# Kernel optimization log

Hardware: AMD Instinct MI355X
Metric: run time of the kernel (lower is better)

## Reference

```python
import jax, jax.numpy as jnp
import numpy as np

B, N, D_IN, D_OUT = 4, 512, 128, 64
TEMP = 1.0
BN_EPS = 1e-5


def setup_inputs() -> dict:
    key = jax.random.key(0)
    ks = jax.random.split(key, 9)
    return {
        "x": jax.random.normal(ks[0], (B, N, D_IN), jnp.float32),
        "att_proj_w": jax.random.normal(ks[1], (D_OUT, D_IN), jnp.float32) * 0.08,
        "att_proj_b": jax.random.normal(ks[2], (D_OUT,), jnp.float32) * 0.01,
        "att_weight": jax.random.normal(ks[3], (D_OUT, 1), jnp.float32) * 0.15,
        "proj_with_att_w": jax.random.normal(ks[4], (D_OUT, D_IN), jnp.float32) * 0.08,
        "proj_with_att_b": jax.random.normal(ks[5], (D_OUT,), jnp.float32) * 0.01,
        "proj_without_att_w": jax.random.normal(ks[6], (D_OUT, D_IN), jnp.float32) * 0.08,
        "proj_without_att_b": jax.random.normal(ks[7], (D_OUT,), jnp.float32) * 0.01,
        "bn_gamma": jnp.ones((D_OUT,), jnp.float32),
        "bn_beta": jnp.zeros((D_OUT,), jnp.float32),
    }


def reference(x, att_proj_w, att_proj_b, att_weight,
              proj_with_att_w, proj_with_att_b,
              proj_without_att_w, proj_without_att_b,
              bn_gamma, bn_beta):
    # Dropout is identity (inference). Pairwise node multiplication: (B,N,N,D_in)
    pair = x[:, :, None, :] * x[:, None, :, :]
    # Linear + tanh on the pairwise tensor -> (B,N,N,D_out)
    a = jnp.tanh(jnp.einsum('bijd,od->bijo', pair, att_proj_w) + att_proj_b)
    # Score via learned vector, temperature, softmax over second node axis (torch dim=-2 of (B,N,N,1))
    scores = jnp.einsum('bijo,o->bij', a, att_weight[:, 0]) / TEMP
    att = jax.nn.softmax(scores, axis=2)  # normalize over j
    # Attention-weighted aggregation + two projections (torch Linear: x @ W.T + b)
    agg = jnp.einsum('bij,bjd->bid', att, x)
    h = (agg @ proj_with_att_w.T + proj_with_att_b) \
        + (x @ proj_without_att_w.T + proj_without_att_b)
    # BatchNorm1d (training-mode batch stats) over flattened (B*N, D_out)
    hf = h.reshape(-1, h.shape[-1])
    mean = hf.mean(axis=0)
    var = hf.var(axis=0)  # biased, as torch BN uses for normalization
    y = (hf - mean) / jnp.sqrt(var + BN_EPS) * bn_gamma + bn_beta
    y = y.reshape(h.shape)
    return jax.nn.selu(y)
```

## Files before the change

### kernel.cpp

```cpp
#include <hip/hip_runtime.h>
#include <math.h>

#define NB 4
#define NN 512
#define DIN 128
#define DOUT 64
#define TI 2
#define CHROWS 32
#define NCH (NN / CHROWS)

typedef __attribute__((ext_vector_type(8))) short short8;
typedef __attribute__((ext_vector_type(8))) unsigned short ushort8;
typedef __attribute__((ext_vector_type(16))) float f32x16;

__device__ __forceinline__ unsigned short f2bf(float f) {
    union { float f; unsigned u; } v; v.f = f;
    unsigned r = v.u + 0x7fffu + ((v.u >> 16) & 1u);
    return (unsigned short)(r >> 16);
}

__device__ __forceinline__ float bf2f(unsigned short u) {
    union { unsigned u; float f; } v; v.u = ((unsigned)u) << 16; return v.f;
}

__global__ void x_to_bf16(const float* __restrict__ x, unsigned short* __restrict__ xbf) {
    const int idx = blockIdx.x * 256 + threadIdx.x;
    float4 v = ((const float4*)x)[idx];
    ushort4 o;
    o.x = f2bf(v.x); o.y = f2bf(v.y); o.z = f2bf(v.z); o.w = f2bf(v.w);
    ((ushort4*)xbf)[idx] = o;
}

__global__ __launch_bounds__(256, 3) void gat_main(
    const float* __restrict__ x,
    const unsigned short* __restrict__ xbf,
    const float* __restrict__ apw,
    const float* __restrict__ apb,
    const float* __restrict__ attw,
    const float* __restrict__ pww,
    const float* __restrict__ pwb,
    const float* __restrict__ pow_,
    const float* __restrict__ pob,
    float* __restrict__ out)
{
    __shared__ unsigned short xt[2][CHROWS * DIN];
    __shared__ float scp[2][TI][NN];
    __shared__ float xis[TI][DIN];
    __shared__ float red_s[4][TI];
    __shared__ float bcs[TI];

    float* pagg = (float*)&xt[0][0];
    float* aggs = pagg + 8 * TI * DIN;
    float* pr   = aggs + TI * DIN;

    const int t = threadIdx.x;
    const int blk = blockIdx.x;
    const int b = blk >> 8;
    const int rowbase = (blk & 255) * TI;
    const float* xb = x + (size_t)b * NN * DIN;
    const unsigned short* xbb = xbf + (size_t)b * NN * DIN;

    {
        const int i = t >> 7, d = t & 127;
        xis[i][d] = xb[(size_t)(rowbase + i) * DIN + d];
    }

    const int lane = t & 63, wid = t >> 6;
    const int qi = wid & 1;
    const int oh = wid >> 1;
    const int l31 = lane & 31;
    const int hi = lane >> 5;

    const int r0 = t >> 4, g0 = t & 15;
    const int st_off0 = r0 * 256 + ((g0 ^ (r0 & 7)) << 4);
    const int r1 = 16 + r0;
    const int st_off1 = r1 * 256 + ((g0 ^ (r1 & 7)) << 4);

    int rdoff[8];
    #pragma unroll
    for (int ks = 0; ks < 8; ++ks)
        rdoff[ks] = l31 * 256 + (((ks * 2 + hi) ^ (l31 & 7)) << 4);

    ushort8 v0a = ((const ushort8*)xbb)[t];
    ushort8 v0b = ((const ushort8*)xbb)[t + 256];
    __syncthreads();

    short8 afr[8];
    {
        const float* wrow = apw + (size_t)(oh * 32 + l31) * DIN;
        const float* xk0 = &xis[qi][0];
        #pragma unroll
        for (int ks = 0; ks < 8; ++ks) {
            const int k0 = ks * 16 + hi * 8;
            float4 w0 = *(const float4*)(wrow + k0);
            float4 w1 = *(const float4*)(wrow + k0 + 4);
            const float* xk = xk0 + k0;
            short8 fr;
            fr[0] = (short)f2bf(w0.x * xk[0]);
            fr[1] = (short)f2bf(w0.y * xk[1]);
            fr[2] = (short)f2bf(w0.z * xk[2]);
            fr[3] = (short)f2bf(w0.w * xk[3]);
            fr[4] = (short)f2bf(w1.x * xk[4]);
            fr[5] = (short)f2bf(w1.y * xk[5]);
            fr[6] = (short)f2bf(w1.z * xk[6]);
            fr[7] = (short)f2bf(w1.w * xk[7]);
            afr[ks] = fr;
        }
    }

    const float C2 = 2.885390081777927f;
    float awm2[16], abc[16], sumw = 0.0f;
    #pragma unroll
    for (int r = 0; r < 16; ++r) {
        const int crow = (r & 3) + 8 * (r >> 2) + 4 * hi;
        const int o = oh * 32 + crow;
        float wv = attw[o], bv = apb[o];
        awm2[r] = -2.0f * wv;
        abc[r] = bv * C2;
        sumw += wv;
    }

    *(ushort8*)((char*)&xt[0][0] + st_off0) = v0a;
    *(ushort8*)((char*)&xt[0][0] + st_off1) = v0b;
    __syncthreads();

    f32x16 accA, accB;

#define COMPUTE(ACC, BUF) do {                                                  \
    f32x16 zz_ = {0.f,0.f,0.f,0.f,0.f,0.f,0.f,0.f,                              \
                  0.f,0.f,0.f,0.f,0.f,0.f,0.f,0.f};                             \
    ACC = zz_;                                                                  \
    _Pragma("unroll")                                                           \
    for (int ks_ = 0; ks_ < 8; ++ks_) {                                         \
        short8 bk_ = *(const short8*)((const char*)&xt[BUF][0] + rdoff[ks_]);   \
        ACC = __builtin_amdgcn_mfma_f32_32x32x16_bf16(afr[ks_], bk_, ACC, 0, 0, 0); \
    }                                                                           \
} while (0)

#define POST(ACC, CH) do {                                                      \
    float sp_ = sumw;                                                           \
    _Pragma("unroll")                                                           \
    for (int r_ = 0; r_ < 16; ++r_) {                                           \
        float arg_ = fmaf(ACC[r_], C2, abc[r_]);                                \
        float u_, rc_;                                                          \
        asm("v_exp_f32 %0, %1" : "=v"(u_) : "v"(arg_));                         \
        float den_ = u_ + 1.0f;                                                 \
        asm("v_rcp_f32 %0, %1" : "=v"(rc_) : "v"(den_));                        \
        sp_ = fmaf(awm2[r_], rc_, sp_);                                         \
    }                                                                           \
    sp_ += __shfl_xor(sp_, 32);                                                 \
    if (lane < 32) scp[oh][qi][(CH) * 32 + l31] = sp_;                          \
} while (0)

    {
        ushort8 va = ((const ushort8*)xbb)[512 + t];
        ushort8 vb = ((const ushort8*)xbb)[512 + t + 256];
        COMPUTE(accA, 0);
        *(ushort8*)((char*)&xt[1][0] + st_off0) = va;
        *(ushort8*)((char*)&xt[1][0] + st_off1) = vb;
        __syncthreads();
    }
    for (int cb = 1; cb <= NCH - 3; cb += 2) {
        {
            ushort8 va = ((const ushort8*)xbb)[(cb + 1) * 512 + t];
            ushort8 vb = ((const ushort8*)xbb)[(cb + 1) * 512 + t + 256];
            COMPUTE(accB, 1);
            POST(accA, cb - 1);
            *(ushort8*)((char*)&xt[0][0] + st_off0) = va;
            *(ushort8*)((char*)&xt[0][0] + st_off1) = vb;
            __syncthreads();
        }
        {
            ushort8 va = ((const ushort8*)xbb)[(cb + 2) * 512 + t];
            ushort8 vb = ((const ushort8*)xbb)[(cb + 2) * 512 + t + 256];
            COMPUTE(accA, 0);
            POST(accB, cb);
            *(ushort8*)((char*)&xt[1][0] + st_off0) = va;
            *(ushort8*)((char*)&xt[1][0] + st_off1) = vb;
            __syncthreads();
        }
    }
    COMPUTE(accB, 1);
    POST(accA, NCH - 2);
    POST(accB, NCH - 1);
    __syncthreads();

    {
        float s00 = scp[0][0][t] + scp[1][0][t];
        float s01 = scp[0][0][t + 256] + scp[1][0][t + 256];
        float s10 = scp[0][1][t] + scp[1][1][t];
        float s11 = scp[0][1][t + 256] + scp[1][1][t + 256];
        float e00 = __expf(s00), e01 = __expf(s01);
        float e10 = __expf(s10), e11 = __expf(s11);
        scp[0][0][t] = e00; scp[0][0][t + 256] = e01;
        scp[0][1][t] = e10; scp[0][1][t + 256] = e11;
        float ss0 = e00 + e01, ss1 = e10 + e11;
        #pragma unroll
        for (int m = 1; m < 64; m <<= 1) {
            ss0 += __shfl_xor(ss0, m);
            ss1 += __shfl_xor(ss1, m);
        }
        if (lane == 0) { red_s[wid][0] = ss0; red_s[wid][1] = ss1; }
    }
    __syncthreads();
    if (t < TI) {
        float sm = red_s[0][t] + red_s[1][t] + red_s[2][t] + red_s[3][t];
        bcs[t] = 1.0f / sm;
    }
    __syncthreads();

    const float* esc0 = &scp[0][0][0];
    const float* esc1 = &scp[0][1][0];
    {
        const int d0 = (t & 31) * 4, q = t >> 5;
        const unsigned short* xc = xbb + d0;
        float a0[4] = {0.f, 0.f, 0.f, 0.f};
        float a1[4] = {0.f, 0.f, 0.f, 0.f};
        #pragma unroll 4
        for (int jj = q * 64; jj < q * 64 + 64; ++jj) {
            ushort4 xv = *(const ushort4*)(xc + (size_t)jj * DIN);
            float e0v = esc0[jj], e1v = esc1[jj];
            float x0 = bf2f(xv.x), x1 = bf2f(xv.y);
            float x2 = bf2f(xv.z), x3 = bf2f(xv.w);
            a0[0] = fmaf(e0v, x0, a0[0]); a0[1] = fmaf(e0v, x1, a0[1]);
            a0[2] = fmaf(e0v, x2, a0[2]); a0[3] = fmaf(e0v, x3, a0[3]);
            a1[0] = fmaf(e1v, x0, a1[0]); a1[1] = fmaf(e1v, x1, a1[1]);
            a1[2] = fmaf(e1v, x2, a1[2]); a1[3] = fmaf(e1v, x3, a1[3]);
        }
        #pragma unroll
        for (int c = 0; c < 4; ++c) {
            pagg[(q * TI + 0) * DIN + d0 + c] = a0[c];
            pagg[(q * TI + 1) * DIN + d0 + c] = a1[c];
        }
    }
    __syncthreads();
    {
        const int i = t >> 7, d = t & 127;
        float s = 0.f;
        #pragma unroll
        for (int q = 0; q < 8; ++q) s += pagg[(q * TI + i) * DIN + d];
        aggs[i * DIN + d] = s * bcs[i];
    }
    __syncthreads();

    {
        const int o = t & 63, pi = t >> 6;
        const int i = pi >> 1, part = pi & 1;
        const float* w1 = pww + (size_t)o * DIN + part * 64;
        const float* w2 = pow_ + (size_t)o * DIN + part * 64;
        const float* ag = aggs + i * DIN + part * 64;
        const float* xr = &xis[i][part * 64];
        float sum = 0.0f;
        #pragma unroll
        for (int dd = 0; dd < 64; ++dd)
            sum += w1[dd] * ag[dd] + w2[dd] * xr[dd];
        pr[pi * DOUT + o] = sum;
    }
    __syncthreads();
    if (t < TI * DOUT) {
        const int i = t >> 6, o = t & 63;
        float h = pr[(i * 2) * DOUT + o] + pr[(i * 2 + 1) * DOUT + o] + pwb[o] + pob[o];
        out[(size_t)(b * NN + rowbase + i) * DOUT + o] = h;
    }
#undef COMPUTE
#undef POST
}

__global__ void bn_stats(const float* __restrict__ h, float* __restrict__ stats) {
    const int c = blockIdx.x;
    const int t = threadIdx.x;
    float s = 0.f, s2 = 0.f;
    for (int r = t; r < NB * NN; r += 256) {
        float v = h[(size_t)r * DOUT + c];
        s += v; s2 += v * v;
    }
    __shared__ float rs[256], rs2[256];
    rs[t] = s; rs2[t] = s2;
    __syncthreads();
    for (int k = 128; k > 0; k >>= 1) {
        if (t < k) { rs[t] += rs[t + k]; rs2[t] += rs2[t + k]; }
        __syncthreads();
    }
    if (t == 0) {
        const float inv_n = 1.0f / (float)(NB * NN);
        float mean = rs[0] * inv_n;
        float var = rs2[0] * inv_n - mean * mean;
        stats[c] = mean;
        stats[DOUT + c] = rsqrtf(var + 1e-5f);
    }
}

__global__ void bn_selu(float* __restrict__ out, const float* __restrict__ stats,
                        const float* __restrict__ gamma, const float* __restrict__ beta) {
    const int idx = blockIdx.x * 256 + threadIdx.x;
    const int c = idx & 63;
    float v = out[idx];
    float y = (v - stats[c]) * stats[DOUT + c] * gamma[c] + beta[c];
    const float scale = 1.0507009873554805f;
    const float alpha = 1.6732632423543772f;
    out[idx] = y > 0.0f ? scale * y : scale * alpha * (__expf(y) - 1.0f);
}

extern "C" void kernel_launch(void* const* d_in, const int* in_sizes, int n_in,
                              void* d_out, int out_size, void* d_ws, size_t ws_size,
                              hipStream_t stream) {
    const float* x    = (const float*)d_in[0];
    const float* apw  = (const float*)d_in[1];
    const float* apb  = (const float*)d_in[2];
    const float* attw = (const float*)d_in[3];
    const float* pww  = (const float*)d_in[4];
    const float* pwb  = (const float*)d_in[5];
    const float* pow_ = (const float*)d_in[6];
    const float* pob  = (const float*)d_in[7];
    const float* gmm  = (const float*)d_in[8];
    const float* bta  = (const float*)d_in[9];
    float* out = (float*)d_out;
    float* stats = (float*)d_ws;
    unsigned short* xbf = (unsigned short*)((char*)d_ws + 1024);

    x_to_bf16<<<256, 256, 0, stream>>>(x, xbf);
    gat_main<<<NB * NN / TI, 256, 0, stream>>>(x, xbf, apw, apb, attw, pww, pwb, pow_, pob, out);
    bn_stats<<<DOUT, 256, 0, stream>>>(out, stats);
    bn_selu<<<(NB * NN * DOUT) / 256, 256, 0, stream>>>(out, stats, gmm, bta);
}
```

Before: 66.74 us.

## Load MFMA B fragments directly from global memory instead of LDS staging

Drops the double-buffered LDS tile of bf16 x rows and the per-chunk barriers. Each lane now loads its MFMA B-operand fragments straight from global memory, one chunk ahead in registers. This removes LDS writes and reads and the synchronisation between chunks. In exchange every wave re-reads the same x chunk from global or L2, register pressure rises with the extra prefetched fragments, and load latency is hidden only by the one-chunk lookahead.

```diff
diff --git a/kernel.cpp b/kernel.cpp
--- a/kernel.cpp
+++ b/kernel.cpp
@@ -10,7 +10,7 @@
 #define NCH (NN / CHROWS)
 
 typedef __attribute__((ext_vector_type(8))) short short8;
-typedef __attribute__((ext_vector_type(8))) unsigned short ushort8;
+typedef __attribute__((ext_vector_type(4))) float f32x4;
 typedef __attribute__((ext_vector_type(16))) float f32x16;
 
 __device__ __forceinline__ unsigned short f2bf(float f) {
@@ -43,15 +43,13 @@
     const float* __restrict__ pob,
     float* __restrict__ out)
 {
-    __shared__ unsigned short xt[2][CHROWS * DIN];
     __shared__ float scp[2][TI][NN];
     __shared__ float xis[TI][DIN];
     __shared__ float red_s[4][TI];
     __shared__ float bcs[TI];
-
-    float* pagg = (float*)&xt[0][0];
-    float* aggs = pagg + 8 * TI * DIN;
-    float* pr   = aggs + TI * DIN;
+    __shared__ float pagg[8][TI][DIN];
+    __shared__ float aggs[TI][DIN];
+    __shared__ float pr[4][DOUT];
 
     const int t = threadIdx.x;
     const int blk = blockIdx.x;
@@ -71,18 +69,17 @@
     const int l31 = lane & 31;
     const int hi = lane >> 5;
 
-    const int r0 = t >> 4, g0 = t & 15;
-    const int st_off0 = r0 * 256 + ((g0 ^ (r0 & 7)) << 4);
-    const int r1 = 16 + r0;
-    const int st_off1 = r1 * 256 + ((g0 ^ (r1 & 7)) << 4);
-
-    int rdoff[8];
-    #pragma unroll
-    for (int ks = 0; ks < 8; ++ks)
-        rdoff[ks] = l31 * 256 + (((ks * 2 + hi) ^ (l31 & 7)) << 4);
-
-    ushort8 v0a = ((const ushort8*)xbb)[t];
-    ushort8 v0b = ((const ushort8*)xbb)[t + 256];
+    const short8* bbase = (const short8*)(xbb + (size_t)l31 * DIN + hi * 8);
+
+#define LOADB(BFR, CH) do {                                                     \
+    const short8* bp_ = bbase + (size_t)(CH) * (CHROWS * DIN / 8);              \
+    _Pragma("unroll")                                                           \
+    for (int ks_ = 0; ks_ < 8; ++ks_) BFR[ks_] = bp_[ks_ * 2];                  \
+} while (0)
+
+    short8 bfr[8];
+    LOADB(bfr, 0);
+
     __syncthreads();
 
     short8 afr[8];
@@ -120,21 +117,15 @@
         sumw += wv;
     }
 
-    *(ushort8*)((char*)&xt[0][0] + st_off0) = v0a;
-    *(ushort8*)((char*)&xt[0][0] + st_off1) = v0b;
-    __syncthreads();
-
     f32x16 accA, accB;
 
-#define COMPUTE(ACC, BUF) do {                                                  \
+#define COMPUTE(ACC, BFR) do {                                                  \
     f32x16 zz_ = {0.f,0.f,0.f,0.f,0.f,0.f,0.f,0.f,                              \
                   0.f,0.f,0.f,0.f,0.f,0.f,0.f,0.f};                             \
     ACC = zz_;                                                                  \
     _Pragma("unroll")                                                           \
-    for (int ks_ = 0; ks_ < 8; ++ks_) {                                         \
-        short8 bk_ = *(const short8*)((const char*)&xt[BUF][0] + rdoff[ks_]);   \
-        ACC = __builtin_amdgcn_mfma_f32_32x32x16_bf16(afr[ks_], bk_, ACC, 0, 0, 0); \
-    }                                                                           \
+    for (int ks_ = 0; ks_ < 8; ++ks_)                                           \
+        ACC = __builtin_amdgcn_mfma_f32_32x32x16_bf16(afr[ks_], BFR[ks_], ACC, 0, 0, 0); \
 } while (0)
 
 #define POST(ACC, CH) do {                                                      \
@@ -152,35 +143,17 @@
     if (lane < 32) scp[oh][qi][(CH) * 32 + l31] = sp_;                          \
 } while (0)
 
-    {
-        ushort8 va = ((const ushort8*)xbb)[512 + t];
-        ushort8 vb = ((const ushort8*)xbb)[512 + t + 256];
-        COMPUTE(accA, 0);
-        *(ushort8*)((char*)&xt[1][0] + st_off0) = va;
-        *(ushort8*)((char*)&xt[1][0] + st_off1) = vb;
-        __syncthreads();
-    }
+    COMPUTE(accA, bfr);
+    LOADB(bfr, 1);
     for (int cb = 1; cb <= NCH - 3; cb += 2) {
-        {
-            ushort8 va = ((const ushort8*)xbb)[(cb + 1) * 512 + t];
-            ushort8 vb = ((const ushort8*)xbb)[(cb + 1) * 512 + t + 256];
-            COMPUTE(accB, 1);
-            POST(accA, cb - 1);
-            *(ushort8*)((char*)&xt[0][0] + st_off0) = va;
-            *(ushort8*)((char*)&xt[0][0] + st_off1) = vb;
-            __syncthreads();
-        }
-        {
-            ushort8 va = ((const ushort8*)xbb)[(cb + 2) * 512 + t];
-            ushort8 vb = ((const ushort8*)xbb)[(cb + 2) * 512 + t + 256];
-            COMPUTE(accA, 0);
-            POST(accB, cb);
-            *(ushort8*)((char*)&xt[1][0] + st_off0) = va;
-            *(ushort8*)((char*)&xt[1][0] + st_off1) = vb;
-            __syncthreads();
-        }
-    }
-    COMPUTE(accB, 1);
+        COMPUTE(accB, bfr);
+        LOADB(bfr, cb + 1);
+        POST(accA, cb - 1);
+        COMPUTE(accA, bfr);
+        LOADB(bfr, cb + 2);
+        POST(accB, cb);
+    }
+    COMPUTE(accB, bfr);
     POST(accA, NCH - 2);
     POST(accB, NCH - 1);
     __syncthreads();
@@ -229,8 +202,8 @@
         }
         #pragma unroll
         for (int c = 0; c < 4; ++c) {
-            pagg[(q * TI + 0) * DIN + d0 + c] = a0[c];
-            pagg[(q * TI + 1) * DIN + d0 + c] = a1[c];
+            pagg[q][0][d0 + c] = a0[c];
+            pagg[q][1][d0 + c] = a1[c];
         }
     }
     __syncthreads();
@@ -238,8 +211,8 @@
         const int i = t >> 7, d = t & 127;
         float s = 0.f;
         #pragma unroll
-        for (int q = 0; q < 8; ++q) s += pagg[(q * TI + i) * DIN + d];
-        aggs[i * DIN + d] = s * bcs[i];
+        for (int q = 0; q < 8; ++q) s += pagg[q][i][d];
+        aggs[i][d] = s * bcs[i];
     }
     __syncthreads();
 
@@ -248,22 +221,23 @@
         const int i = pi >> 1, part = pi & 1;
         const float* w1 = pww + (size_t)o * DIN + part * 64;
         const float* w2 = pow_ + (size_t)o * DIN + part * 64;
-        const float* ag = aggs + i * DIN + part * 64;
+        const float* ag = &aggs[i][part * 64];
         const float* xr = &xis[i][part * 64];
         float sum = 0.0f;
         #pragma unroll
         for (int dd = 0; dd < 64; ++dd)
             sum += w1[dd] * ag[dd] + w2[dd] * xr[dd];
-        pr[pi * DOUT + o] = sum;
+        pr[pi][o] = sum;
     }
     __syncthreads();
     if (t < TI * DOUT) {
         const int i = t >> 6, o = t & 63;
-        float h = pr[(i * 2) * DOUT + o] + pr[(i * 2 + 1) * DOUT + o] + pwb[o] + pob[o];
+        float h = pr[i * 2][o] + pr[i * 2 + 1][o] + pwb[o] + pob[o];
         out[(size_t)(b * NN + rowbase + i) * DOUT + o] = h;
     }
 #undef COMPUTE
 #undef POST
+#undef LOADB
 }
 
 __global__ void bn_stats(const float* __restrict__ h, float* __restrict__ stats) {
```

New measurement: 106.1 us. 59.0% more time.

## Split attention reduction over key halves and add combine-projection kernel

Applied to the files above, without the earlier changes.

Each row pair is now processed by two blocks, each covering half of the j (key) range. Each block writes unnormalized partial aggregation sums and softmax denominators to workspace. A new combine_proj kernel adds the partials, normalizes, and applies both linear projections. This is meant to raise block count and reduce tail imbalance in the main kernel. It costs a duplicated per-block setup, extra global memory traffic and an extra kernel launch.

```diff
diff --git a/kernel.cpp b/kernel.cpp
--- a/kernel.cpp
+++ b/kernel.cpp
@@ -7,7 +7,8 @@
 #define DOUT 64
 #define TI 2
 #define CHROWS 32
-#define NCH (NN / CHROWS)
+#define NCHL 8
+#define NTOT (NB * NN)
 
 typedef __attribute__((ext_vector_type(8))) short short8;
 typedef __attribute__((ext_vector_type(8))) unsigned short ushort8;
@@ -37,26 +38,23 @@
     const float* __restrict__ apw,
     const float* __restrict__ apb,
     const float* __restrict__ attw,
-    const float* __restrict__ pww,
-    const float* __restrict__ pwb,
-    const float* __restrict__ pow_,
-    const float* __restrict__ pob,
-    float* __restrict__ out)
+    float* __restrict__ pnum,
+    float* __restrict__ pden)
 {
     __shared__ unsigned short xt[2][CHROWS * DIN];
-    __shared__ float scp[2][TI][NN];
+    __shared__ float scp[2][TI][256];
     __shared__ float xis[TI][DIN];
     __shared__ float red_s[4][TI];
-    __shared__ float bcs[TI];
 
     float* pagg = (float*)&xt[0][0];
-    float* aggs = pagg + 8 * TI * DIN;
-    float* pr   = aggs + TI * DIN;
 
     const int t = threadIdx.x;
     const int blk = blockIdx.x;
-    const int b = blk >> 8;
-    const int rowbase = (blk & 255) * TI;
+    const int jh = blk & 1;
+    const int rp = blk >> 1;
+    const int b = rp >> 8;
+    const int rowbase = (rp & 255) * TI;
+    const int rid0 = rp * TI;
     const float* xb = x + (size_t)b * NN * DIN;
     const unsigned short* xbb = xbf + (size_t)b * NN * DIN;
 
@@ -81,8 +79,8 @@
     for (int ks = 0; ks < 8; ++ks)
         rdoff[ks] = l31 * 256 + (((ks * 2 + hi) ^ (l31 & 7)) << 4);
 
-    ushort8 v0a = ((const ushort8*)xbb)[t];
-    ushort8 v0b = ((const ushort8*)xbb)[t + 256];
+    ushort8 v0a = ((const ushort8*)xbb)[(jh * NCHL) * 512 + t];
+    ushort8 v0b = ((const ushort8*)xbb)[(jh * NCHL) * 512 + t + 256];
     __syncthreads();
 
     short8 afr[8];
@@ -152,49 +150,44 @@
     if (lane < 32) scp[oh][qi][(CH) * 32 + l31] = sp_;                          \
 } while (0)
 
-    {
-        ushort8 va = ((const ushort8*)xbb)[512 + t];
-        ushort8 vb = ((const ushort8*)xbb)[512 + t + 256];
+#define STAGE(BUF, CH) do {                                                     \
+    ushort8 va_ = ((const ushort8*)xbb)[(jh * NCHL + (CH)) * 512 + t];          \
+    ushort8 vb_ = ((const ushort8*)xbb)[(jh * NCHL + (CH)) * 512 + t + 256];    \
+    *(ushort8*)((char*)&xt[BUF][0] + st_off0) = va_;                            \
+    *(ushort8*)((char*)&xt[BUF][0] + st_off1) = vb_;                            \
+} while (0)
+
+    {
         COMPUTE(accA, 0);
-        *(ushort8*)((char*)&xt[1][0] + st_off0) = va;
-        *(ushort8*)((char*)&xt[1][0] + st_off1) = vb;
+        STAGE(1, 1);
         __syncthreads();
     }
-    for (int cb = 1; cb <= NCH - 3; cb += 2) {
+    for (int cb = 1; cb <= NCHL - 3; cb += 2) {
         {
-            ushort8 va = ((const ushort8*)xbb)[(cb + 1) * 512 + t];
-            ushort8 vb = ((const ushort8*)xbb)[(cb + 1) * 512 + t + 256];
             COMPUTE(accB, 1);
             POST(accA, cb - 1);
-            *(ushort8*)((char*)&xt[0][0] + st_off0) = va;
-            *(ushort8*)((char*)&xt[0][0] + st_off1) = vb;
+            STAGE(0, cb + 1);
             __syncthreads();
         }
         {
-            ushort8 va = ((const ushort8*)xbb)[(cb + 2) * 512 + t];
-            ushort8 vb = ((const ushort8*)xbb)[(cb + 2) * 512 + t + 256];
             COMPUTE(accA, 0);
             POST(accB, cb);
-            *(ushort8*)((char*)&xt[1][0] + st_off0) = va;
-            *(ushort8*)((char*)&xt[1][0] + st_off1) = vb;
+            STAGE(1, cb + 2);
             __syncthreads();
         }
     }
     COMPUTE(accB, 1);
-    POST(accA, NCH - 2);
-    POST(accB, NCH - 1);
-    __syncthreads();
-
-    {
-        float s00 = scp[0][0][t] + scp[1][0][t];
-        float s01 = scp[0][0][t + 256] + scp[1][0][t + 256];
-        float s10 = scp[0][1][t] + scp[1][1][t];
-        float s11 = scp[0][1][t + 256] + scp[1][1][t + 256];
-        float e00 = __expf(s00), e01 = __expf(s01);
-        float e10 = __expf(s10), e11 = __expf(s11);
-        scp[0][0][t] = e00; scp[0][0][t + 256] = e01;
-        scp[0][1][t] = e10; scp[0][1][t + 256] = e11;
-        float ss0 = e00 + e01, ss1 = e10 + e11;
+    POST(accA, NCHL - 2);
+    POST(accB, NCHL - 1);
+    __syncthreads();
+
+    {
+        float s0 = scp[0][0][t] + scp[1][0][t];
+        float s1 = scp[0][1][t] + scp[1][1][t];
+        float e0 = __expf(s0), e1 = __expf(s1);
+        scp[0][0][t] = e0;
+        scp[0][1][t] = e1;
+        float ss0 = e0, ss1 = e1;
         #pragma unroll
         for (int m = 1; m < 64; m <<= 1) {
             ss0 += __shfl_xor(ss0, m);
@@ -204,20 +197,19 @@
     }
     __syncthreads();
     if (t < TI) {
-        float sm = red_s[0][t] + red_s[1][t] + red_s[2][t] + red_s[3][t];
-        bcs[t] = 1.0f / sm;
-    }
-    __syncthreads();
+        float den = red_s[0][t] + red_s[1][t] + red_s[2][t] + red_s[3][t];
+        pden[jh * NTOT + rid0 + t] = den;
+    }
 
     const float* esc0 = &scp[0][0][0];
     const float* esc1 = &scp[0][1][0];
     {
         const int d0 = (t & 31) * 4, q = t >> 5;
-        const unsigned short* xc = xbb + d0;
+        const unsigned short* xc = xbb + (size_t)(jh * 256) * DIN + d0;
         float a0[4] = {0.f, 0.f, 0.f, 0.f};
         float a1[4] = {0.f, 0.f, 0.f, 0.f};
         #pragma unroll 4
-        for (int jj = q * 64; jj < q * 64 + 64; ++jj) {
+        for (int jj = q * 32; jj < q * 32 + 32; ++jj) {
             ushort4 xv = *(const ushort4*)(xc + (size_t)jj * DIN);
             float e0v = esc0[jj], e1v = esc1[jj];
             float x0 = bf2f(xv.x), x1 = bf2f(xv.y);
@@ -239,38 +231,49 @@
         float s = 0.f;
         #pragma unroll
         for (int q = 0; q < 8; ++q) s += pagg[(q * TI + i) * DIN + d];
-        aggs[i * DIN + d] = s * bcs[i];
-    }
-    __syncthreads();
-
-    {
-        const int o = t & 63, pi = t >> 6;
-        const int i = pi >> 1, part = pi & 1;
-        const float* w1 = pww + (size_t)o * DIN + part * 64;
-        const float* w2 = pow_ + (size_t)o * DIN + part * 64;
-        const float* ag = aggs + i * DIN + part * 64;
-        const float* xr = &xis[i][part * 64];
-        float sum = 0.0f;
-        #pragma unroll
-        for (int dd = 0; dd < 64; ++dd)
-            sum += w1[dd] * ag[dd] + w2[dd] * xr[dd];
-        pr[pi * DOUT + o] = sum;
-    }
-    __syncthreads();
-    if (t < TI * DOUT) {
-        const int i = t >> 6, o = t & 63;
-        float h = pr[(i * 2) * DOUT + o] + pr[(i * 2 + 1) * DOUT + o] + pwb[o] + pob[o];
-        out[(size_t)(b * NN + rowbase + i) * DOUT + o] = h;
+        pnum[(size_t)(jh * NTOT + rid0 + i) * DIN + d] = s;
     }
 #undef COMPUTE
 #undef POST
+#undef STAGE
+}
+
+__global__ __launch_bounds__(256) void combine_proj(
+    const float* __restrict__ x,
+    const float* __restrict__ pnum, const float* __restrict__ pden,
+    const float* __restrict__ pww, const float* __restrict__ pwb,
+    const float* __restrict__ pow_, const float* __restrict__ pob,
+    float* __restrict__ out)
+{
+    __shared__ float aggL[4][DIN];
+    __shared__ float xiL[4][DIN];
+    const int t = threadIdx.x, lane = t & 63, w = t >> 6;
+    const int rid = blockIdx.x * 4 + w;
+    {
+        const int d = lane;
+        float inv = 1.0f / (pden[rid] + pden[NTOT + rid]);
+        float n0 = pnum[(size_t)rid * DIN + d] + pnum[(size_t)(NTOT + rid) * DIN + d];
+        float n1 = pnum[(size_t)rid * DIN + d + 64] + pnum[(size_t)(NTOT + rid) * DIN + d + 64];
+        aggL[w][d] = n0 * inv;
+        aggL[w][d + 64] = n1 * inv;
+        xiL[w][d] = x[(size_t)rid * DIN + d];
+        xiL[w][d + 64] = x[(size_t)rid * DIN + d + 64];
+    }
+    const int o = lane;
+    const float* w1 = pww + (size_t)o * DIN;
+    const float* w2 = pow_ + (size_t)o * DIN;
+    float sum = 0.0f;
+    #pragma unroll 8
+    for (int dd = 0; dd < DIN; ++dd)
+        sum += w1[dd] * aggL[w][dd] + w2[dd] * xiL[w][dd];
+    out[(size_t)rid * DOUT + o] = sum + pwb[o] + pob[o];
 }
 
 __global__ void bn_stats(const float* __restrict__ h, float* __restrict__ stats) {
     const int c = blockIdx.x;
     const int t = threadIdx.x;
     float s = 0.f, s2 = 0.f;
-    for (int r = t; r < NB * NN; r += 256) {
+    for (int r = t; r < NTOT; r += 256) {
         float v = h[(size_t)r * DOUT + c];
         s += v; s2 += v * v;
     }
@@ -282,7 +285,7 @@
         __syncthreads();
     }
     if (t == 0) {
-        const float inv_n = 1.0f / (float)(NB * NN);
+        const float inv_n = 1.0f / (float)NTOT;
         float mean = rs[0] * inv_n;
         float var = rs2[0] * inv_n - mean * mean;
         stats[c] = mean;
@@ -315,11 +318,16 @@
     const float* gmm  = (const float*)d_in[8];
     const float* bta  = (const float*)d_in[9];
     float* out = (float*)d_out;
-    float* stats = (float*)d_ws;
-    unsigned short* xbf = (unsigned short*)((char*)d_ws + 1024);
+
+    char* ws = (char*)d_ws;
+    float* stats = (float*)ws;
+    unsigned short* xbf = (unsigned short*)(ws + 1024);
+    float* pnum = (float*)(ws + 528384);
+    float* pden = (float*)(ws + 528384 + 2097152);
 
     x_to_bf16<<<256, 256, 0, stream>>>(x, xbf);
-    gat_main<<<NB * NN / TI, 256, 0, stream>>>(x, xbf, apw, apb, attw, pww, pwb, pow_, pob, out);
+    gat_main<<<2 * NTOT / TI, 256, 0, stream>>>(x, xbf, apw, apb, attw, pnum, pden);
+    combine_proj<<<NTOT / 4, 256, 0, stream>>>(x, pnum, pden, pww, pwb, pow_, pob, out);
     bn_stats<<<DOUT, 256, 0, stream>>>(out, stats);
-    bn_selu<<<(NB * NN * DOUT) / 256, 256, 0, stream>>>(out, stats, gmm, bta);
-}
+    bn_selu<<<(NTOT * DOUT) / 256, 256, 0, stream>>>(out, stats, gmm, bta);
+}
```

Result: slower. 77.08 us (+15.5%).
